# Kernel optimization log

Measured on AMD Instinct MI355X. Metric: run time of the kernel, lower is better.

Reference implementation:

```python
import jax, jax.numpy as jnp
import numpy as np
from jax import lax

ALIGNED_H = 7
ALIGNED_W = 7
SPATIAL_SCALE = 0.125
B, C, H, W = 4, 512, 96, 96
R = 512
IMG = 768  # image resolution (features are image/8)


def setup_inputs() -> dict:
    key = jax.random.key(0)
    k1, k2, k3, k4, k5, k6 = jax.random.split(key, 6)
    features = jax.random.normal(k1, (B, C, H, W), dtype=jnp.float32)
    # realistic rois: [batch_idx, x1, y1, x2, y2] in image coordinates
    bi = jax.random.randint(k2, (R,), 0, B).astype(jnp.float32)
    cx = jax.random.uniform(k3, (R,), minval=32.0, maxval=float(IMG - 32))
    cy = jax.random.uniform(k4, (R,), minval=32.0, maxval=float(IMG - 32))
    bw = jax.random.uniform(k5, (R,), minval=16.0, maxval=256.0)
    bh = jax.random.uniform(k6, (R,), minval=16.0, maxval=256.0)
    x1 = jnp.clip(cx - bw / 2, 0.0, IMG - 1.0)
    x2 = jnp.clip(cx + bw / 2, 0.0, IMG - 1.0)
    y1 = jnp.clip(cy - bh / 2, 0.0, IMG - 1.0)
    y2 = jnp.clip(cy + bh / 2, 0.0, IMG - 1.0)
    rois = jnp.stack([bi, x1, y1, x2, y2], axis=1)
    return {"features": features, "rois": rois}


def _roi_align_ada(features, rois, ah, aw, scale):
    """RoIAlignAda: per output pixel, average of a 3x3 adaptive-stride grid of
    bilinear samples centered at the bin point (RT-MDNet ROIAlignAdaForward)."""
    b, c, h, w = features.shape
    r = rois.shape[0]
    batch_ind = rois[:, 0].astype(jnp.int32)
    x1 = rois[:, 1] * scale
    y1 = rois[:, 2] * scale
    x2 = rois[:, 3] * scale
    y2 = rois[:, 4] * scale
    roi_w = jnp.maximum(x2 - x1, 0.0)
    roi_h = jnp.maximum(y2 - y1, 0.0)
    bin_h = roi_h / (ah - 1.0)  # [R]
    bin_w = roi_w / (aw - 1.0)
    ph = jnp.arange(ah, dtype=jnp.float32)
    pw = jnp.arange(aw, dtype=jnp.float32)
    hc = y1[:, None] + ph[None, :] * bin_h[:, None]  # [R, AH] bin centers
    wc = x1[:, None] + pw[None, :] * bin_w[:, None]  # [R, AW]
    stride_h = jnp.maximum(1.0, jnp.round(bin_h / 3.0))  # [R]
    stride_w = jnp.maximum(1.0, jnp.round(bin_w / 3.0))

    center_ok = ((hc >= 0) & (hc < h))[:, :, None] & ((wc >= 0) & (wc < w))[:, None, :]  # [R,AH,AW]

    # flatten spatial for gathers: [B*H*W, C]
    f = features.transpose(0, 2, 3, 1).reshape(b * h * w, c)
    base = batch_ind[:, None, None] * (h * w)  # [R,1,1]

    acc = jnp.zeros((r, ah, aw, c), dtype=features.dtype)
    cnt = jnp.zeros((r, ah, aw), dtype=features.dtype)
    for sh in (-1.0, 0.0, 1.0):
        for sw in (-1.0, 0.0, 1.0):
            ch = hc + sh * stride_h[:, None]  # [R,AH]
            cw = wc + sw * stride_w[:, None]  # [R,AW]
            valid = ((ch >= 0) & (ch < h))[:, :, None] & ((cw >= 0) & (cw < w))[:, None, :]
            hs = jnp.clip(jnp.floor(ch), 0.0, h - 2.0)
            ws = jnp.clip(jnp.floor(cw), 0.0, w - 2.0)
            hr = (ch - hs)[:, :, None]  # [R,AH,1]
            wr = (cw - ws)[:, None, :] * jnp.ones((r, ah, aw), features.dtype)[:, :1, :1]  # broadcast helper
            wr = (cw - ws)[:, None, :]  # [R,1,AW]
            hsi = hs.astype(jnp.int32)[:, :, None]  # [R,AH,1]
            wsi = ws.astype(jnp.int32)[:, None, :]  # [R,1,AW]
            ul = base + hsi * w + wsi  # [R,AH,AW]
            v = (f[ul] * ((1.0 - hr) * (1.0 - wr))[..., None]
                 + f[ul + 1] * ((1.0 - hr) * wr)[..., None]
                 + f[ul + w] * (hr * (1.0 - wr))[..., None]
                 + f[ul + w + 1] * (hr * wr)[..., None])  # [R,AH,AW,C]
            acc = acc + jnp.where(valid[..., None], v, 0.0)
            cnt = cnt + valid.astype(features.dtype)

    out = jnp.where(center_ok[..., None], acc / jnp.maximum(cnt, 1.0)[..., None], 0.0)
    return out.transpose(0, 3, 1, 2)  # [R, C, AH, AW]


def reference(features, rois):
    x = _roi_align_ada(features, rois, ALIGNED_H + 4, ALIGNED_W + 4, SPATIAL_SCALE)  # [R,C,11,11]
    # fused 3x3 stride-2 max pool -> [R, C, 5, 5]
    out = lax.reduce_window(x, -jnp.inf, lax.max,
                            window_dimensions=(1, 1, 3, 3),
                            window_strides=(1, 1, 2, 2),
                            padding='VALID')
    return out
```

## Files before the change

### kernel.cpp

```cpp
#include <hip/hip_runtime.h>
#include <stdint.h>

typedef unsigned short u16;
typedef unsigned int   u32;

#define Bn 4
#define Cc 512
#define Hh 96
#define Ww 96
#define HWc (Hh*Ww)
#define AH 11
#define Rr 512
#define CP (Cc/2)

__device__ __forceinline__ u16 f2bf(float f){
  u32 u = __float_as_uint(f);
  u += 0x7fffu + ((u>>16)&1u);
  return (u16)(u>>16);
}
__device__ __forceinline__ u32 pk2(float a, float b){
  return (u32)f2bf(a) | ((u32)f2bf(b)<<16);
}

__global__ __launch_bounds__(256)
void transpose_kernel(const float* __restrict__ in, u32* __restrict__ out){
  __shared__ u32 tile[128*64];
  const int t = threadIdx.x;
  const int hw0 = blockIdx.x*128, c0 = blockIdx.y*128, b = blockIdx.z;
  {
    const int q = t & 31, cp0 = t >> 5;
    const float* ib = in + ((size_t)(b*Cc + c0))*HWc + hw0 + 4*q;
    #pragma unroll
    for (int p=0;p<8;++p){
      const int cp = cp0 + p*8;
      const float* pa = ib + (size_t)(2*cp)*HWc;
      float4 A = *(const float4*)pa;
      float4 B = *(const float4*)(pa + HWc);
      const int cs = cp ^ q;
      tile[(4*q+0)*64 + cs] = pk2(A.x,B.x);
      tile[(4*q+1)*64 + cs] = pk2(A.y,B.y);
      tile[(4*q+2)*64 + cs] = pk2(A.z,B.z);
      tile[(4*q+3)*64 + cs] = pk2(A.w,B.w);
    }
  }
  __syncthreads();
  {
    const int l = t & 63, wv = t >> 6;
    u32* ob = out + ((size_t)b*HWc + hw0)*CP + (c0>>1) + l;
    #pragma unroll
    for (int k=0;k<32;++k){
      const int hw = wv*32 + k;
      ob[(size_t)hw*CP] = tile[hw*64 + (l ^ (hw>>2))];
    }
  }
}

__global__ __launch_bounds__(512)
void roi_sort(const float* __restrict__ rois, int* __restrict__ idx){
  __shared__ int cnt[4], off[4], cur[4];
  const int t = threadIdx.x;
  int b = min(max((int)rois[t*5], 0), Bn-1);
  if (t < 4){ cnt[t] = 0; }
  __syncthreads();
  atomicAdd(&cnt[b], 1);
  __syncthreads();
  if (t == 0){
    int o = 0;
    for (int i=0;i<4;++i){ off[i]=o; cur[i]=o; o+=cnt[i]; }
  }
  __syncthreads();
  int pos = atomicAdd(&cur[b], 1);
  idx[8+pos] = t;
  if (t < 4){ idx[t] = cnt[t]; idx[4+t] = off[t]; }
}

__device__ __forceinline__ float2 bilin(const u32 v[16], const float cw[4], const float rw[4]){
  float ax=0.0f, ay=0.0f;
  #pragma unroll
  for (int i=0;i<4;++i){
    float cx=0.0f, cy=0.0f;
    #pragma unroll
    for (int j=0;j<4;++j){
      u32 d = v[i*4+j];
      cx = fmaf(cw[j], __uint_as_float(d<<16),           cx);
      cy = fmaf(cw[j], __uint_as_float(d & 0xffff0000u), cy);
    }
    ax = fmaf(rw[i], cx, ax);
    ay = fmaf(rw[i], cy, ay);
  }
  return make_float2(ax, ay);
}

__global__ __launch_bounds__(128)
void roi_align_max_nhwc(const u32* __restrict__ feat,
                        const float* __restrict__ rois,
                        float* __restrict__ out,
                        const int* __restrict__ idx)
{
  __shared__ __align__(16) int4   s_ro[AH];
  __shared__ __align__(16) float4 s_rw[AH];
  __shared__ __align__(16) int4   s_co[AH];
  __shared__ __align__(16) float4 s_cw[AH];
  __shared__ int s_b;
  __shared__ __align__(16) float s_out[256*25];

  const int t   = threadIdx.x;
  const int bid = blockIdx.x;

  int r, half;
  if (idx){
    const int k = bid & 7;
    const int j = bid >> 3;
    const int b = k >> 1;
    half = k & 1;
    const int cntb = idx[b];
    if (j < cntb && j < 128){
      r = idx[8 + idx[4+b] + j];
    } else {
      int dr = 0;
      for (int b2=0; b2<b; ++b2) dr += max(0, 128 - idx[b2]);
      dr += j - min(cntb, 128);
      int acc = 0; r = 0;
      for (int b2=0; b2<4; ++b2){
        int ex = max(0, idx[b2] - 128);
        if (dr < acc + ex){ r = idx[8 + idx[4+b2] + 128 + (dr - acc)]; break; }
        acc += ex;
      }
    }
  } else {
    r = bid >> 1; half = bid & 1;
  }

  if (t == 0){
    int b = (int)rois[r*5+0];
    s_b = min(max(b, 0), Bn-1);
  }

  if (t < AH || (t >= 64 && t < 64+AH)){
    const bool isrow = (t < AH);
    const int  p = isrow ? t : t-64;
    const float* rp = rois + r*5;
    const float c1 = rp[isrow?2:1], c2 = rp[isrow?4:3];
    float lo  = __fmul_rn(c1, 0.125f);
    float hi  = __fmul_rn(c2, 0.125f);
    float ext = fmaxf(__fsub_rn(hi,lo), 0.0f);
    float bin = __fdiv_rn(ext, 10.0f);
    float ctr = __fadd_rn(lo, __fmul_rn((float)p, bin));
    float strd = fmaxf(1.0f, rintf(__fdiv_rn(bin, 3.0f)));
    bool ok = (ctr >= 0.0f) && (ctr < 96.0f);
    int rws[6]; float wts[6]; int nv=0;
    #pragma unroll
    for (int s=0;s<3;++s){
      float cc = __fadd_rn(ctr, __fmul_rn((float)(s-1), strd));
      bool vv = (cc >= 0.0f) && (cc < 96.0f);
      float fl = fminf(fmaxf(floorf(cc),0.0f),94.0f);
      float fr = __fsub_rn(cc, fl);
      int ri = (int)fl;
      rws[2*s]=ri; rws[2*s+1]=ri+1;
      wts[2*s]  = vv ? __fsub_rn(1.0f,fr) : 0.0f;
      wts[2*s+1]= vv ? fr : 0.0f;
      nv += vv?1:0;
    }
    float sc = ok ? (1.0f/(float)nv) : 0.0f;
    int cr[4]={0,0,0,0}; float cwv[4]={0.0f,0.0f,0.0f,0.0f}; int n=0;
    for (int k=0;k<6;++k){
      float wk=wts[k]; if (wk==0.0f) continue;
      int rr=rws[k]; bool fnd=false;
      for (int j=0;j<n;++j) if (cr[j]==rr){ cwv[j]+=wk; fnd=true; break; }
      if (!fnd && n<4){ cr[n]=rr; cwv[n]=wk; ++n; }
    }
    const int mul = isrow ? (Ww*CP*4) : (CP*4);
    if (isrow){
      s_ro[p] = make_int4(cr[0]*mul, cr[1]*mul, cr[2]*mul, cr[3]*mul);
      s_rw[p] = make_float4(cwv[0]*sc, cwv[1]*sc, cwv[2]*sc, cwv[3]*sc);
    } else {
      s_co[p] = make_int4(cr[0]*mul, cr[1]*mul, cr[2]*mul, cr[3]*mul);
      s_cw[p] = make_float4(cwv[0]*sc, cwv[1]*sc, cwv[2]*sc, cwv[3]*sc);
    }
  }
  __syncthreads();

  const char* fb = (const char*)(feat + (size_t)s_b*((size_t)HWc*CP));
  const int tb4 = (half*128 + t)*4;

  int   vo[AH][4]; float cwr[AH][4];
  #pragma unroll
  for (int pw=0; pw<AH; ++pw){
    int4 c4 = s_co[pw]; float4 w4 = s_cw[pw];
    vo[pw][0]=tb4+c4.x; vo[pw][1]=tb4+c4.y; vo[pw][2]=tb4+c4.z; vo[pw][3]=tb4+c4.w;
    cwr[pw][0]=w4.x; cwr[pw][1]=w4.y; cwr[pw][2]=w4.z; cwr[pw][3]=w4.w;
  }

  float2 awin[5];
  #pragma unroll 1
  for (int ph=0; ph<AH; ++ph){
    int4   r4 = s_ro[ph];
    float4 w4 = s_rw[ph];
    const char* r0 = fb + __builtin_amdgcn_readfirstlane(r4.x);
    const char* r1 = fb + __builtin_amdgcn_readfirstlane(r4.y);
    const char* r2 = fb + __builtin_amdgcn_readfirstlane(r4.z);
    const char* r3 = fb + __builtin_amdgcn_readfirstlane(r4.w);
    const float rw_[4] = {w4.x, w4.y, w4.z, w4.w};
    float2 binr[AH];
    u32 va[16], vb[16], vc[16];

#define LDV(dst, PW) do{                              \
    dst[ 0] = *(const u32*)(r0 + vo[PW][0]);          \
    dst[ 1] = *(const u32*)(r0 + vo[PW][1]);          \
    dst[ 2] = *(const u32*)(r0 + vo[PW][2]);          \
    dst[ 3] = *(const u32*)(r0 + vo[PW][3]);          \
    dst[ 4] = *(const u32*)(r1 + vo[PW][0]);          \
    dst[ 5] = *(const u32*)(r1 + vo[PW][1]);          \
    dst[ 6] = *(const u32*)(r1 + vo[PW][2]);          \
    dst[ 7] = *(const u32*)(r1 + vo[PW][3]);          \
    dst[ 8] = *(const u32*)(r2 + vo[PW][0]);          \
    dst[ 9] = *(const u32*)(r2 + vo[PW][1]);          \
    dst[10] = *(const u32*)(r2 + vo[PW][2]);          \
    dst[11] = *(const u32*)(r2 + vo[PW][3]);          \
    dst[12] = *(const u32*)(r3 + vo[PW][0]);          \
    dst[13] = *(const u32*)(r3 + vo[PW][1]);          \
    dst[14] = *(const u32*)(r3 + vo[PW][2]);          \
    dst[15] = *(const u32*)(r3 + vo[PW][3]);          \
  }while(0)
#define CMP(src, PW) binr[PW] = bilin(src, cwr[PW], rw_)

    LDV(va, 0); LDV(vb, 1); LDV(vc, 2);
    CMP(va, 0); LDV(va, 3);
    CMP(vb, 1); LDV(vb, 4);
    CMP(vc, 2); LDV(vc, 5);
    CMP(va, 3); LDV(va, 6);
    CMP(vb, 4); LDV(vb, 7);
    CMP(vc, 5); LDV(vc, 8);
    CMP(va, 6); LDV(va, 9);
    CMP(vb, 7); LDV(vb, 10);
    CMP(vc, 8);
    CMP(va, 9);
    CMP(vb, 10);
#undef LDV
#undef CMP

    float2 rm[5];
    #pragma unroll
    for (int ox=0; ox<5; ++ox){
      rm[ox].x = fmaxf(fmaxf(binr[2*ox].x, binr[2*ox+1].x), binr[2*ox+2].x);
      rm[ox].y = fmaxf(fmaxf(binr[2*ox].y, binr[2*ox+1].y), binr[2*ox+2].y);
    }
    if (ph == 0){
      #pragma unroll
      for (int ox=0; ox<5; ++ox) awin[ox] = rm[ox];
    } else if (ph & 1){
      #pragma unroll
      for (int ox=0; ox<5; ++ox){
        awin[ox].x = fmaxf(awin[ox].x, rm[ox].x);
        awin[ox].y = fmaxf(awin[ox].y, rm[ox].y);
      }
    } else {
      const int oy = (ph-2) >> 1;
      #pragma unroll
      for (int ox=0; ox<5; ++ox){
        s_out[(2*t  )*25 + oy*5 + ox] = fmaxf(awin[ox].x, rm[ox].x);
        s_out[(2*t+1)*25 + oy*5 + ox] = fmaxf(awin[ox].y, rm[ox].y);
        awin[ox] = rm[ox];
      }
    }
  }
  __syncthreads();

  float4* dst = (float4*)(out + (size_t)r*(Cc*25) + half*(256*25));
  const float4* src = (const float4*)s_out;
  for (int k=t; k<(256*25)/4; k+=128) dst[k]=src[k];
}

__global__ __launch_bounds__(512, 1)
void roi_align_max_nchw(const float* __restrict__ feat,
                        const float* __restrict__ rois,
                        float* __restrict__ out)
{
  __shared__ int   s_roff[AH][6];
  __shared__ float s_rw  [AH][6];
  __shared__ int   s_coff[AH][6];
  __shared__ float s_cw  [AH][6];
  __shared__ int   s_b;
  __shared__ __align__(16) float s_out[Cc*25];

  const int t = threadIdx.x;
  const int r = blockIdx.x;

  if (t < AH*6){
    ((float*)s_rw)[t] = 0.0f;  ((int*)s_roff)[t] = 0;
    ((float*)s_cw)[t] = 0.0f;  ((int*)s_coff)[t] = 0;
  }
  if (t == 0){
    int b = (int)rois[r*5+0];
    s_b = min(max(b, 0), Bn-1);
  }
  __syncthreads();

  if (t < AH || (t >= 64 && t < 64+AH)){
    const bool isrow = (t < AH);
    const int  p = isrow ? t : t-64;
    const float* rp = rois + r*5;
    const float c1 = rp[isrow?2:1], c2 = rp[isrow?4:3];
    float lo  = __fmul_rn(c1, 0.125f);
    float hi  = __fmul_rn(c2, 0.125f);
    float ext = fmaxf(__fsub_rn(hi,lo), 0.0f);
    float bin = __fdiv_rn(ext, 10.0f);
    float ctr = __fadd_rn(lo, __fmul_rn((float)p, bin));
    float strd = fmaxf(1.0f, rintf(__fdiv_rn(bin, 3.0f)));
    bool ok = (ctr >= 0.0f) && (ctr < 96.0f);
    int rws[6]; float wts[6]; int nv=0;
    #pragma unroll
    for (int s=0;s<3;++s){
      float cc = __fadd_rn(ctr, __fmul_rn((float)(s-1), strd));
      bool vv = (cc >= 0.0f) && (cc < 96.0f);
      float fl = fminf(fmaxf(floorf(cc),0.0f),94.0f);
      float fr = __fsub_rn(cc, fl);
      int ri = (int)fl;
      rws[2*s]=ri; rws[2*s+1]=ri+1;
      wts[2*s]  = vv ? __fsub_rn(1.0f,fr) : 0.0f;
      wts[2*s+1]= vv ? fr : 0.0f;
      nv += vv?1:0;
    }
    float sc = ok ? (1.0f/(float)nv) : 0.0f;
    int cr[6]; float cw[6]; int n=0;
    for (int k=0;k<6;++k){
      float wk=wts[k]; if (wk==0.0f) continue;
      if (n>0 && cr[n-1]==rws[k]) cw[n-1]+=wk;
      else { cr[n]=rws[k]; cw[n]=wk; ++n; }
    }
    const int mul = isrow ? Ww : 1;
    for (int k=0;k<n;++k){
      int off = cr[k]*mul;
      float wv = cw[k]*sc;
      if (isrow){ s_roff[p][k]=off; s_rw[p][k]=wv; }
      else      { s_coff[p][k]=off; s_cw[p][k]=wv; }
    }
  }
  __syncthreads();

  const float* f0 = feat + ((size_t)s_b*Cc + t)*HWc;
  float awin[5];
  for (int ph=0; ph<AH; ++ph){
    float binrow[AH];
    #pragma unroll
    for (int pw=0; pw<AH; ++pw){
      float acc = 0.0f;
      #pragma unroll
      for (int ai=0; ai<6; ++ai){
        float ra = s_rw[ph][ai];
        if (ra == 0.0f) continue;
        int ro = s_roff[ph][ai];
        #pragma unroll
        for (int bi=0; bi<6; ++bi){
          float cb = s_cw[pw][bi];
          if (cb == 0.0f) continue;
          acc = fmaf(ra*cb, f0[ro + s_coff[pw][bi]], acc);
        }
      }
      binrow[pw] = acc;
    }
    float rm[5];
    #pragma unroll
    for (int ox=0; ox<5; ++ox)
      rm[ox] = fmaxf(fmaxf(binrow[2*ox], binrow[2*ox+1]), binrow[2*ox+2]);
    if (ph == 0){
      #pragma unroll
      for (int ox=0; ox<5; ++ox) awin[ox] = rm[ox];
    } else if (ph & 1){
      #pragma unroll
      for (int ox=0; ox<5; ++ox) awin[ox] = fmaxf(awin[ox], rm[ox]);
    } else {
      int oy = (ph-2) >> 1;
      #pragma unroll
      for (int ox=0; ox<5; ++ox){
        s_out[t*25 + oy*5 + ox] = fmaxf(awin[ox], rm[ox]);
        awin[ox] = rm[ox];
      }
    }
  }
  __syncthreads();

  float4* dst = (float4*)(out + (size_t)r*(Cc*25));
  const float4* src = (const float4*)s_out;
  for (int k=t; k<(Cc*25)/4; k+=512) dst[k]=src[k];
}

extern "C" void kernel_launch(void* const* d_in, const int* in_sizes, int n_in,
                              void* d_out, int out_size, void* d_ws, size_t ws_size,
                              hipStream_t stream)
{
  (void)in_sizes; (void)n_in; (void)out_size;
  const float* feat = (const float*)d_in[0];
  const float* rois = (const float*)d_in[1];
  float* out = (float*)d_out;
  const size_t need = (size_t)Bn*HWc*Cc*sizeof(u16);
  if (ws_size >= need){
    u32* ws = (u32*)d_ws;
    int* idx = nullptr;
    if (ws_size >= need + 4096){
      idx = (int*)((char*)d_ws + need);
      roi_sort<<<1, 512, 0, stream>>>(rois, idx);
    }
    dim3 g(HWc/128, Cc/128, Bn);
    transpose_kernel<<<g, 256, 0, stream>>>(feat, ws);
    roi_align_max_nhwc<<<Rr*2, 128, 0, stream>>>(ws, rois, out, idx);
  } else {
    roi_align_max_nchw<<<Rr, 512, 0, stream>>>(feat, rois, out);
  }
}
```

Measured before the change: 164.0 us.

## Fold ROI sort into transpose, vectorize transpose stores, deepen gather pipeline

Merges the single-block ROI bucketing kernel into the first block of the transpose kernel, which removes one kernel launch. The transpose write-back now reads and writes 16-byte uint4 chunks and undoes the XOR swizzle with lane permutations, in place of scalar 4-byte stores. The bilinear gather loop in the ROI-align kernel now keeps four load buffers in flight instead of three, which raises register pressure. These are several unrelated changes made at once.

```diff
diff --git a/kernel.cpp b/kernel.cpp
--- a/kernel.cpp
+++ b/kernel.cpp
@@ -23,7 +23,8 @@
 }
 
 __global__ __launch_bounds__(256)
-void transpose_kernel(const float* __restrict__ in, u32* __restrict__ out){
+void transpose_kernel(const float* __restrict__ in, u32* __restrict__ out,
+                      const float* __restrict__ rois, int* __restrict__ idx){
   __shared__ u32 tile[128*64];
   const int t = threadIdx.x;
   const int hw0 = blockIdx.x*128, c0 = blockIdx.y*128, b = blockIdx.z;
@@ -46,32 +47,41 @@
   __syncthreads();
   {
     const int l = t & 63, wv = t >> 6;
-    u32* ob = out + ((size_t)b*HWc + hw0)*CP + (c0>>1) + l;
-    #pragma unroll
-    for (int k=0;k<32;++k){
-      const int hw = wv*32 + k;
-      ob[(size_t)hw*CP] = tile[hw*64 + (l ^ (hw>>2))];
-    }
-  }
-}
-
-__global__ __launch_bounds__(512)
-void roi_sort(const float* __restrict__ rois, int* __restrict__ idx){
-  __shared__ int cnt[4], off[4], cur[4];
-  const int t = threadIdx.x;
-  int b = min(max((int)rois[t*5], 0), Bn-1);
-  if (t < 4){ cnt[t] = 0; }
-  __syncthreads();
-  atomicAdd(&cnt[b], 1);
-  __syncthreads();
-  if (t == 0){
-    int o = 0;
-    for (int i=0;i<4;++i){ off[i]=o; cur[i]=o; o+=cnt[i]; }
-  }
-  __syncthreads();
-  int pos = atomicAdd(&cur[b], 1);
-  idx[8+pos] = t;
-  if (t < 4){ idx[t] = cnt[t]; idx[4+t] = off[t]; }
+    const int rsub = l >> 4, q = l & 15;
+    u32* ob = out + ((size_t)b*HWc + hw0)*CP + (c0>>1);
+    #pragma unroll
+    for (int k=0;k<8;++k){
+      const int hw = wv*32 + k*4 + rsub;
+      const int s  = hw >> 2;
+      const int m  = s & 3;
+      const u32* tp = &tile[hw*64 + ((4*q) ^ (s & ~3))];
+      uint4 R = *(const uint4*)tp;
+      uint4 W;
+      if      (m==0) W = R;
+      else if (m==1) W = make_uint4(R.y,R.x,R.w,R.z);
+      else if (m==2) W = make_uint4(R.z,R.w,R.x,R.y);
+      else           W = make_uint4(R.w,R.z,R.y,R.x);
+      *(uint4*)(ob + (size_t)hw*CP + 4*q) = W;
+    }
+  }
+  if (idx && blockIdx.x==0 && blockIdx.y==0 && blockIdx.z==0){
+    __shared__ int cnt[4], off[4], cur[4];
+    if (t < 4) cnt[t] = 0;
+    __syncthreads();
+    int b0 = min(max((int)rois[t*5], 0), Bn-1);
+    int b1 = min(max((int)rois[(t+256)*5], 0), Bn-1);
+    atomicAdd(&cnt[b0], 1);
+    atomicAdd(&cnt[b1], 1);
+    __syncthreads();
+    if (t == 0){
+      int o = 0;
+      for (int i=0;i<4;++i){ off[i]=o; cur[i]=o; o+=cnt[i]; }
+    }
+    __syncthreads();
+    int p0 = atomicAdd(&cur[b0], 1); idx[8+p0] = t;
+    int p1 = atomicAdd(&cur[b1], 1); idx[8+p1] = t+256;
+    if (t < 4){ idx[t] = cnt[t]; idx[4+t] = off[t]; }
+  }
 }
 
 __device__ __forceinline__ float2 bilin(const u32 v[16], const float cw[4], const float rw[4]){
@@ -202,7 +212,7 @@
     const char* r3 = fb + __builtin_amdgcn_readfirstlane(r4.w);
     const float rw_[4] = {w4.x, w4.y, w4.z, w4.w};
     float2 binr[AH];
-    u32 va[16], vb[16], vc[16];
+    u32 va[16], vb[16], vc[16], vd[16];
 
 #define LDV(dst, PW) do{                              \
     dst[ 0] = *(const u32*)(r0 + vo[PW][0]);          \
@@ -224,18 +234,18 @@
   }while(0)
 #define CMP(src, PW) binr[PW] = bilin(src, cwr[PW], rw_)
 
-    LDV(va, 0); LDV(vb, 1); LDV(vc, 2);
-    CMP(va, 0); LDV(va, 3);
-    CMP(vb, 1); LDV(vb, 4);
-    CMP(vc, 2); LDV(vc, 5);
-    CMP(va, 3); LDV(va, 6);
-    CMP(vb, 4); LDV(vb, 7);
-    CMP(vc, 5); LDV(vc, 8);
-    CMP(va, 6); LDV(va, 9);
-    CMP(vb, 7); LDV(vb, 10);
-    CMP(vc, 8);
-    CMP(va, 9);
-    CMP(vb, 10);
+    LDV(va, 0); LDV(vb, 1); LDV(vc, 2); LDV(vd, 3);
+    CMP(va, 0); LDV(va, 4);
+    CMP(vb, 1); LDV(vb, 5);
+    CMP(vc, 2); LDV(vc, 6);
+    CMP(vd, 3); LDV(vd, 7);
+    CMP(va, 4); LDV(va, 8);
+    CMP(vb, 5); LDV(vb, 9);
+    CMP(vc, 6); LDV(vc, 10);
+    CMP(vd, 7);
+    CMP(va, 8);
+    CMP(vb, 9);
+    CMP(vc, 10);
 #undef LDV
 #undef CMP
 
@@ -397,12 +407,9 @@
   if (ws_size >= need){
     u32* ws = (u32*)d_ws;
     int* idx = nullptr;
-    if (ws_size >= need + 4096){
-      idx = (int*)((char*)d_ws + need);
-      roi_sort<<<1, 512, 0, stream>>>(rois, idx);
-    }
+    if (ws_size >= need + 4096) idx = (int*)((char*)d_ws + need);
     dim3 g(HWc/128, Cc/128, Bn);
-    transpose_kernel<<<g, 256, 0, stream>>>(feat, ws);
+    transpose_kernel<<<g, 256, 0, stream>>>(feat, ws, rois, idx);
     roi_align_max_nhwc<<<Rr*2, 128, 0, stream>>>(ws, rois, out, idx);
   } else {
     roi_align_max_nchw<<<Rr, 512, 0, stream>>>(feat, rois, out);
```

New measurement: 161.9 us. About the same (-1.3%).
